# Kernel optimization log

Hardware: AMD Instinct MI355X
Metric: run time of the kernel (lower is better)

## Reference

```python
import jax, jax.numpy as jnp
import numpy as np

CLASSES = 1000
M = 64   # input_features
N_OUT = 64  # output_features
B = 4
L = 8192


def setup_inputs() -> dict:
    key = jax.random.key(0)
    k1, k2, k3, k4 = jax.random.split(key, 4)
    k = float(np.sqrt(1.0 / M))
    x = jax.random.normal(k1, (B, M, L), dtype=jnp.float32)
    inds = jax.random.randint(k2, (B, L), 0, CLASSES, dtype=jnp.int64)
    # torch.rand(...)*2k - k  -> uniform in [-k, k]
    w = jax.random.uniform(k3, (CLASSES, M, N_OUT), dtype=jnp.float32, minval=-k, maxval=k)
    b = jax.random.uniform(k4, (CLASSES, 1, N_OUT), dtype=jnp.float32, minval=-k, maxval=k)
    return {"x": x, "inds": inds, "w": w, "b": b}


def reference(x, inds, w, b):
    # x: [B, m, L]  (channel-first, like torch)
    Bb, m, Ll = x.shape
    xt = jnp.swapaxes(x, 1, 2).reshape(-1, m)          # [N, m], N = B*L
    idx = inds.reshape(-1)                              # [N]
    w_g = w[idx]                                        # [N, m, n] gathered per-sample weights
    b_g = b[idx, 0]                                     # [N, n]
    out = jnp.einsum('nm,nmo->no', xt, w_g) + b_g       # [N, n]
    out = out.reshape(Bb, Ll, -1)                       # [B, L, n]
    return jnp.swapaxes(out, 1, 2)                      # [B, n, L]
```

## Files before the change

### kernel.cpp

```cpp
#include <hip/hip_runtime.h>


#define M_DIM 64
#define N_OUTD 64
#define L_DIM 8192
#define B_DIM 4
#define NCLS 1000
#define NSAMP (B_DIM * L_DIM)

typedef float float4v __attribute__((ext_vector_type(4)));
typedef int   int4v   __attribute__((ext_vector_type(4)));

#define XG_OFF   0ull
#define OTB_OFF  8388608ull
#define RANK_OFF 16777216ull
#define OFFS_OFF 16908288ull
#define CUR_OFF  16912384ull
#define WS_NEED  16916384ull

__global__ __launch_bounds__(1024) void k_binprep(
    const int* __restrict__ inds, int* __restrict__ offs, int* __restrict__ cur) {
  __shared__ int h[1024];
  __shared__ int s[1024];
  const int tid = threadIdx.x;
  h[tid] = 0;
  __syncthreads();
  const int4v* ip = (const int4v*)inds;
#pragma unroll
  for (int r = 0; r < NSAMP / 4 / 1024; ++r) {
    int4v v = ip[r * 1024 + tid];
    atomicAdd(&h[v.x], 1); atomicAdd(&h[v.y], 1);
    atomicAdd(&h[v.z], 1); atomicAdd(&h[v.w], 1);
  }
  __syncthreads();
  const int v = h[tid];
  s[tid] = v;
  __syncthreads();
  for (int off = 1; off < 1024; off <<= 1) {
    int t = (tid >= off) ? s[tid - off] : 0;
    __syncthreads();
    s[tid] += t;
    __syncthreads();
  }
  if (tid < NCLS) {
    const int excl = s[tid] - v;
    offs[tid] = excl;
    cur[tid]  = excl;
  }
  if (tid == NCLS - 1) offs[NCLS] = s[tid];
}

__global__ __launch_bounds__(256) void k_tin_scatter(
    const float* __restrict__ x, const int* __restrict__ inds,
    int* __restrict__ cur, float* __restrict__ xg, int* __restrict__ rank) {
  __shared__ float tile[64][68];
  __shared__ int posv[64];
  const int tid = threadIdx.x;
  const int b  = blockIdx.x >> 7;
  const int l0 = (blockIdx.x & 127) << 6;

  if (tid < 64) {
    const int n = b * L_DIM + l0 + tid;
    const int pos = atomicAdd(&cur[inds[n]], 1);
    posv[tid] = pos;
    rank[n] = pos;
  }

  const float* xb = x + ((size_t)b * M_DIM) * L_DIM + l0;
  const int r  = tid >> 4;
  const int c4 = (tid & 15) * 4;
#pragma unroll
  for (int p = 0; p < 4; ++p) {
    const int m = r + 16 * p;
    float4v v = *(const float4v*)(xb + (size_t)m * L_DIM + c4);
#pragma unroll
    for (int q = 0; q < 4; ++q) tile[c4 + q][m] = v[q];
  }
  __syncthreads();
#pragma unroll
  for (int p = 0; p < 4; ++p) {
    const int li = r + 16 * p;
    float4v v = *(const float4v*)(&tile[li][c4]);
    *(float4v*)(xg + (size_t)posv[li] * M_DIM + c4) = v;
  }
}

__global__ __launch_bounds__(256) void k_main(
    const float* __restrict__ xg, const int* __restrict__ offs,
    const float* __restrict__ w, const float* __restrict__ bias,
    float* __restrict__ otb) {
  __shared__ float wl[4096];
  __shared__ float xs[64][68];

  const int tid = threadIdx.x;
  const int c   = blockIdx.x;
  const int start = offs[c];
  const int count = offs[c + 1] - start;

  const float* wp = w + (size_t)c * (M_DIM * N_OUTD);
#pragma unroll
  for (int p = 0; p < 4; ++p) {
    const int idx = (p * 256 + tid) * 4;
    *(float4v*)(&wl[idx]) = *(const float4v*)(wp + idx);
  }

  const int wid  = tid >> 6;
  const int lane = tid & 63;
  const int G    = wid * 4 + (lane >> 4);
  const int oi   = (lane & 15) * 4;
  const int jb   = G * 4;

  const float4v bv = *(const float4v*)(bias + (size_t)c * N_OUTD + oi);

  for (int s0 = 0; s0 < count; s0 += 64) {
    __syncthreads();
#pragma unroll
    for (int p = 0; p < 4; ++p) {
      const int idx = p * 256 + tid;
      const int row = idx >> 4;
      const int c4  = (idx & 15) * 4;
      if (s0 + row < count)
        *(float4v*)(&xs[row][c4]) = *(const float4v*)(xg + (size_t)(start + s0 + row) * M_DIM + c4);
    }
    __syncthreads();

    if (s0 + jb < count) {
      float4v a0 = bv, a1 = bv, a2 = bv, a3 = bv;
#pragma unroll 8
      for (int m = 0; m < M_DIM; ++m) {
        const float4v wv = *(const float4v*)(&wl[m * N_OUTD + oi]);
        a0 += xs[jb + 0][m] * wv;
        a1 += xs[jb + 1][m] * wv;
        a2 += xs[jb + 2][m] * wv;
        a3 += xs[jb + 3][m] * wv;
      }
      float* ob = otb + (size_t)(start + s0 + jb) * N_OUTD + oi;
      *(float4v*)(ob) = a0;
      if (s0 + jb + 1 < count) *(float4v*)(ob + 1 * N_OUTD) = a1;
      if (s0 + jb + 2 < count) *(float4v*)(ob + 2 * N_OUTD) = a2;
      if (s0 + jb + 3 < count) *(float4v*)(ob + 3 * N_OUTD) = a3;
    }
  }
}

__global__ __launch_bounds__(256) void k_tout(
    const float* __restrict__ otb, const int* __restrict__ rank,
    float* __restrict__ out) {
  __shared__ float tile[64][68];
  __shared__ int rk[64];
  const int tid = threadIdx.x;
  const int b  = blockIdx.x >> 7;
  const int l0 = (blockIdx.x & 127) << 6;

  if (tid < 64) rk[tid] = rank[b * L_DIM + l0 + tid];
  __syncthreads();

  const int r  = tid >> 4;
  const int c4 = (tid & 15) * 4;
#pragma unroll
  for (int p = 0; p < 4; ++p) {
    const int li = r + 16 * p;
    float4v v = *(const float4v*)(otb + (size_t)rk[li] * N_OUTD + c4);
#pragma unroll
    for (int q = 0; q < 4; ++q) tile[c4 + q][li] = v[q];
  }
  __syncthreads();
  float* ob = out + ((size_t)b * N_OUTD) * L_DIM + l0;
#pragma unroll
  for (int p = 0; p < 4; ++p) {
    const int o = r + 16 * p;
    float4v v = *(const float4v*)(&tile[o][c4]);
    *(float4v*)(ob + (size_t)o * L_DIM + c4) = v;
  }
}

#define TL 16
__global__ __launch_bounds__(256) void condmul_fallback(
    const float* __restrict__ x, const int* __restrict__ inds,
    const float* __restrict__ w, const float* __restrict__ bias,
    float* __restrict__ out) {
  __shared__ float xs[M_DIM][TL];
  __shared__ float os[TL][N_OUTD + 4];
  const int tid  = threadIdx.x;
  const int wid  = tid >> 6;
  const int lane = tid & 63;
  const int g    = lane >> 4;
  const int oi   = (lane & 15) * 4;
  const int n0   = blockIdx.x * TL;
  const int b    = n0 / L_DIM;
  const int l0   = n0 % L_DIM;
  {
    const int li = tid & (TL - 1);
    const int m0 = tid >> 4;
    const float* xb = x + ((size_t)b * M_DIM) * L_DIM + l0;
#pragma unroll
    for (int p = 0; p < 4; ++p) {
      const int m = p * 16 + m0;
      xs[m][li] = xb[(size_t)m * L_DIM + li];
    }
  }
  __syncthreads();
  const int li = wid * 4 + g;
  const int c  = inds[n0 + li];
  const float* wp = w + ((size_t)c * M_DIM) * N_OUTD + oi;
  float4v acc = {0.f, 0.f, 0.f, 0.f};
#pragma unroll 8
  for (int m = 0; m < M_DIM; ++m) {
    const float  xv = xs[m][li];
    const float4v wv = *(const float4v*)(wp + (size_t)m * N_OUTD);
    acc += xv * wv;
  }
  acc += *(const float4v*)(bias + (size_t)c * N_OUTD + oi);
  *(float4v*)(&os[li][oi]) = acc;
  __syncthreads();
  {
    const int lo = tid & (TL - 1);
    const int o0 = tid >> 4;
    float* ob = out + ((size_t)b * N_OUTD) * L_DIM + l0;
#pragma unroll
    for (int p = 0; p < 4; ++p) {
      const int o = p * 16 + o0;
      ob[(size_t)o * L_DIM + lo] = os[lo][o];
    }
  }
}

extern "C" void kernel_launch(void* const* d_in, const int* in_sizes, int n_in,
                              void* d_out, int out_size, void* d_ws, size_t ws_size,
                              hipStream_t stream) {
  const float* x    = (const float*)d_in[0];
  const int*   inds = (const int*)d_in[1];
  const float* w    = (const float*)d_in[2];
  const float* bias = (const float*)d_in[3];
  float*       out  = (float*)d_out;

  if (ws_size < WS_NEED) {
    condmul_fallback<<<NSAMP / TL, 256, 0, stream>>>(x, inds, w, bias, out);
    return;
  }

  char* ws = (char*)d_ws;
  float* xg   = (float*)(ws + XG_OFF);
  float* otb  = (float*)(ws + OTB_OFF);
  int*   rank = (int*)(ws + RANK_OFF);
  int*   offs = (int*)(ws + OFFS_OFF);
  int*   cur  = (int*)(ws + CUR_OFF);

  k_binprep<<<1, 1024, 0, stream>>>(inds, offs, cur);
  k_tin_scatter<<<512, 256, 0, stream>>>(x, inds, cur, xg, rank);
  k_main<<<NCLS, 256, 0, stream>>>(xg, offs, w, bias, otb);
  k_tout<<<512, 256, 0, stream>>>(otb, rank, out);
}
```

Baseline: 37.74 us.

## Replace global binning pass with per-class index scan inside main kernel

Drops the single-block histogram/prefix-scan kernel and the atomic scatter into class-sorted buffers. Each class block now scans the whole index array itself, builds a shared-memory list of its sample indices, gathers x rows from a plainly transposed buffer, and writes outputs back in sample order. This removes a serialized one-block launch and the rank indirection in the transpose kernels. In exchange, every block re-reads all indices, and classes with more than 512 samples would be silently truncated by the fixed shared-memory list.

```diff
diff --git a/kernel.cpp b/kernel.cpp
--- a/kernel.cpp
+++ b/kernel.cpp
@@ -7,65 +7,22 @@
 #define B_DIM 4
 #define NCLS 1000
 #define NSAMP (B_DIM * L_DIM)
+#define NSMAX 512
 
 typedef float float4v __attribute__((ext_vector_type(4)));
 typedef int   int4v   __attribute__((ext_vector_type(4)));
 
-#define XG_OFF   0ull
-#define OTB_OFF  8388608ull
-#define RANK_OFF 16777216ull
-#define OFFS_OFF 16908288ull
-#define CUR_OFF  16912384ull
-#define WS_NEED  16916384ull
-
-__global__ __launch_bounds__(1024) void k_binprep(
-    const int* __restrict__ inds, int* __restrict__ offs, int* __restrict__ cur) {
-  __shared__ int h[1024];
-  __shared__ int s[1024];
-  const int tid = threadIdx.x;
-  h[tid] = 0;
-  __syncthreads();
-  const int4v* ip = (const int4v*)inds;
-#pragma unroll
-  for (int r = 0; r < NSAMP / 4 / 1024; ++r) {
-    int4v v = ip[r * 1024 + tid];
-    atomicAdd(&h[v.x], 1); atomicAdd(&h[v.y], 1);
-    atomicAdd(&h[v.z], 1); atomicAdd(&h[v.w], 1);
-  }
-  __syncthreads();
-  const int v = h[tid];
-  s[tid] = v;
-  __syncthreads();
-  for (int off = 1; off < 1024; off <<= 1) {
-    int t = (tid >= off) ? s[tid - off] : 0;
-    __syncthreads();
-    s[tid] += t;
-    __syncthreads();
-  }
-  if (tid < NCLS) {
-    const int excl = s[tid] - v;
-    offs[tid] = excl;
-    cur[tid]  = excl;
-  }
-  if (tid == NCLS - 1) offs[NCLS] = s[tid];
-}
-
-__global__ __launch_bounds__(256) void k_tin_scatter(
-    const float* __restrict__ x, const int* __restrict__ inds,
-    int* __restrict__ cur, float* __restrict__ xg, int* __restrict__ rank) {
+#define XT_OFF   0ull
+#define OT_OFF   8388608ull
+#define WS_NEED  16777216ull
+
+__global__ __launch_bounds__(256) void k_tin(
+    const float* __restrict__ x, float* __restrict__ xt) {
   __shared__ float tile[64][68];
-  __shared__ int posv[64];
   const int tid = threadIdx.x;
   const int b  = blockIdx.x >> 7;
   const int l0 = (blockIdx.x & 127) << 6;
 
-  if (tid < 64) {
-    const int n = b * L_DIM + l0 + tid;
-    const int pos = atomicAdd(&cur[inds[n]], 1);
-    posv[tid] = pos;
-    rank[n] = pos;
-  }
-
   const float* xb = x + ((size_t)b * M_DIM) * L_DIM + l0;
   const int r  = tid >> 4;
   const int c4 = (tid & 15) * 4;
@@ -77,50 +34,70 @@
     for (int q = 0; q < 4; ++q) tile[c4 + q][m] = v[q];
   }
   __syncthreads();
+  float* xtb = xt + ((size_t)(b * L_DIM + l0)) * M_DIM;
 #pragma unroll
   for (int p = 0; p < 4; ++p) {
     const int li = r + 16 * p;
     float4v v = *(const float4v*)(&tile[li][c4]);
-    *(float4v*)(xg + (size_t)posv[li] * M_DIM + c4) = v;
+    *(float4v*)(xtb + (size_t)li * M_DIM + c4) = v;
   }
 }
 
 __global__ __launch_bounds__(256) void k_main(
-    const float* __restrict__ xg, const int* __restrict__ offs,
+    const float* __restrict__ xt, const int* __restrict__ inds,
     const float* __restrict__ w, const float* __restrict__ bias,
-    float* __restrict__ otb) {
+    float* __restrict__ ot) {
   __shared__ float wl[4096];
   __shared__ float xs[64][68];
+  __shared__ int   ns[NSMAX];
+  __shared__ int   scnt;
 
   const int tid = threadIdx.x;
   const int c   = blockIdx.x;
-  const int start = offs[c];
-  const int count = offs[c + 1] - start;
 
   const float* wp = w + (size_t)c * (M_DIM * N_OUTD);
-#pragma unroll
-  for (int p = 0; p < 4; ++p) {
-    const int idx = (p * 256 + tid) * 4;
-    *(float4v*)(&wl[idx]) = *(const float4v*)(wp + idx);
-  }
+  float4v wr[4];
+#pragma unroll
+  for (int p = 0; p < 4; ++p)
+    wr[p] = *(const float4v*)(wp + (size_t)(p * 256 + tid) * 4);
+
+  if (tid == 0) scnt = 0;
+  __syncthreads();
+
+  const int4v* ip = (const int4v*)inds;
+  for (int i = tid; i < NSAMP / 4; i += 256) {
+    const int4v v = ip[i];
+    const int n0 = i * 4;
+    if (v.x == c) { int k = atomicAdd(&scnt, 1); if (k < NSMAX) ns[k] = n0; }
+    if (v.y == c) { int k = atomicAdd(&scnt, 1); if (k < NSMAX) ns[k] = n0 + 1; }
+    if (v.z == c) { int k = atomicAdd(&scnt, 1); if (k < NSMAX) ns[k] = n0 + 2; }
+    if (v.w == c) { int k = atomicAdd(&scnt, 1); if (k < NSMAX) ns[k] = n0 + 3; }
+  }
+
+#pragma unroll
+  for (int p = 0; p < 4; ++p)
+    *(float4v*)(&wl[(p * 256 + tid) * 4]) = wr[p];
+  __syncthreads();
+
+  const int count = scnt;
+  if (count == 0) return;
 
   const int wid  = tid >> 6;
   const int lane = tid & 63;
   const int G    = wid * 4 + (lane >> 4);
   const int oi   = (lane & 15) * 4;
   const int jb   = G * 4;
-
   const float4v bv = *(const float4v*)(bias + (size_t)c * N_OUTD + oi);
 
   for (int s0 = 0; s0 < count; s0 += 64) {
-    __syncthreads();
 #pragma unroll
     for (int p = 0; p < 4; ++p) {
       const int idx = p * 256 + tid;
       const int row = idx >> 4;
       const int c4  = (idx & 15) * 4;
       if (s0 + row < count)
-        *(float4v*)(&xs[row][c4]) = *(const float4v*)(xg + (size_t)(start + s0 + row) * M_DIM + c4);
+        *(float4v*)(&xs[row][c4]) =
+            *(const float4v*)(xt + (size_t)ns[s0 + row] * M_DIM + c4);
     }
     __syncthreads();
 
@@ -134,33 +111,32 @@
         a2 += xs[jb + 2][m] * wv;
         a3 += xs[jb + 3][m] * wv;
       }
-      float* ob = otb + (size_t)(start + s0 + jb) * N_OUTD + oi;
-      *(float4v*)(ob) = a0;
-      if (s0 + jb + 1 < count) *(float4v*)(ob + 1 * N_OUTD) = a1;
-      if (s0 + jb + 2 < count) *(float4v*)(ob + 2 * N_OUTD) = a2;
-      if (s0 + jb + 3 < count) *(float4v*)(ob + 3 * N_OUTD) = a3;
-    }
+      *(float4v*)(ot + (size_t)ns[s0 + jb] * N_OUTD + oi) = a0;
+      if (s0 + jb + 1 < count)
+        *(float4v*)(ot + (size_t)ns[s0 + jb + 1] * N_OUTD + oi) = a1;
+      if (s0 + jb + 2 < count)
+        *(float4v*)(ot + (size_t)ns[s0 + jb + 2] * N_OUTD + oi) = a2;
+      if (s0 + jb + 3 < count)
+        *(float4v*)(ot + (size_t)ns[s0 + jb + 3] * N_OUTD + oi) = a3;
+    }
+    __syncthreads();
   }
 }
 
 __global__ __launch_bounds__(256) void k_tout(
-    const float* __restrict__ otb, const int* __restrict__ rank,
-    float* __restrict__ out) {
+    const float* __restrict__ ot, float* __restrict__ out) {
   __shared__ float tile[64][68];
-  __shared__ int rk[64];
   const int tid = threadIdx.x;
   const int b  = blockIdx.x >> 7;
   const int l0 = (blockIdx.x & 127) << 6;
 
-  if (tid < 64) rk[tid] = rank[b * L_DIM + l0 + tid];
-  __syncthreads();
-
+  const float* otb = ot + ((size_t)(b * L_DIM + l0)) * N_OUTD;
   const int r  = tid >> 4;
   const int c4 = (tid & 15) * 4;
 #pragma unroll
   for (int p = 0; p < 4; ++p) {
     const int li = r + 16 * p;
-    float4v v = *(const float4v*)(otb + (size_t)rk[li] * N_OUTD + c4);
+    float4v v = *(const float4v*)(otb + (size_t)li * N_OUTD + c4);
 #pragma unroll
     for (int q = 0; q < 4; ++q) tile[c4 + q][li] = v[q];
   }
@@ -240,14 +216,10 @@
   }
 
   char* ws = (char*)d_ws;
-  float* xg   = (float*)(ws + XG_OFF);
-  float* otb  = (float*)(ws + OTB_OFF);
-  int*   rank = (int*)(ws + RANK_OFF);
-  int*   offs = (int*)(ws + OFFS_OFF);
-  int*   cur  = (int*)(ws + CUR_OFF);
-
-  k_binprep<<<1, 1024, 0, stream>>>(inds, offs, cur);
-  k_tin_scatter<<<512, 256, 0, stream>>>(x, inds, cur, xg, rank);
-  k_main<<<NCLS, 256, 0, stream>>>(xg, offs, w, bias, otb);
-  k_tout<<<512, 256, 0, stream>>>(otb, rank, out);
-}
+  float* xt = (float*)(ws + XT_OFF);
+  float* ot = (float*)(ws + OT_OFF);
+
+  k_tin<<<512, 256, 0, stream>>>(x, xt);
+  k_main<<<NCLS, 256, 0, stream>>>(xt, inds, w, bias, ot);
+  k_tout<<<512, 256, 0, stream>>>(ot, out);
+}
```

Result: no change. 37.48 us (-0.7%).
